# Optimization experiments

Hardware: AMD Instinct MI355X
Metric: run time of the kernel (lower is better)

Reference implementation:

```python
import jax, jax.numpy as jnp
import numpy as np

B, N, D, WIN = 2, 4096, 256, 16


def setup_inputs() -> dict:
    key = jax.random.key(0)
    ks = jax.random.split(key, 10)
    def lin(k, o, i):
        return 0.02 * jax.random.normal(k, (o, i), jnp.float32)
    W = N // WIN
    return {
        "x": 0.5 * jax.random.normal(ks[0], (B, N, D), jnp.float32),
        "embed_qk": jax.random.normal(ks[1], (3, B, W, WIN, WIN, 3), jnp.float32),
        "act_proj_w": lin(ks[2], D, D), "act_proj_b": jnp.zeros((D,), jnp.float32),
        "proj_ln_g": jnp.ones((D,), jnp.float32), "proj_ln_b": jnp.zeros((D,), jnp.float32),
        "conv_w": lin(ks[3], D, D), "conv_b": jnp.zeros((D,), jnp.float32),
        "q_w": lin(ks[4], D, D), "q_b": jnp.zeros((D,), jnp.float32),
        "k_w": lin(ks[5], D, D), "k_b": jnp.zeros((D,), jnp.float32),
        "p_w": lin(ks[6], 1, 3), "p_b": jnp.zeros((1,), jnp.float32),
        "lin_w": lin(ks[7], D, D), "lin_b": jnp.zeros((D,), jnp.float32),
        "norm_g": jnp.ones((D,), jnp.float32), "norm_b": jnp.zeros((D,), jnp.float32),
    }


def _ln(x, g, b, eps=1e-5):
    m = x.mean(-1, keepdims=True)
    v = ((x - m) ** 2).mean(-1, keepdims=True)
    return (x - m) * jax.lax.rsqrt(v + eps) * g + b


def reference(x, embed_qk, act_proj_w, act_proj_b, proj_ln_g, proj_ln_b,
              conv_w, conv_b, q_w, q_b, k_w, k_b, p_w, p_b,
              lin_w, lin_b, norm_g, norm_b):
    # MSMAttentionLayer: gated residual path
    act_res = jax.nn.silu(x @ act_proj_w.T + act_proj_b)          # (B,N,C)
    h = _ln(x, proj_ln_g, proj_ln_b)
    h = jax.nn.silu(h @ conv_w.T + conv_b)                        # 1x1 conv == per-token linear

    # MSMLMultiHeadAttention, stage=1 (window 4x4=16); N % 16 == 0 so add_row_num = 0
    q = jax.nn.elu(h @ q_w.T + q_b) + 1.0
    k = jax.nn.elu(h @ k_w.T + k_b) + 1.0
    v = h
    Bn, Nn, C = h.shape
    Wn = Nn // WIN
    q_win = q.reshape(Bn, Wn, WIN, C)
    k_win = k.reshape(Bn, Wn, WIN, C)
    v_win = v.reshape(Bn, Wn, WIN, C)
    # learned relative-position bias: Linear(3,1) on embed_qk[stage]
    p = (embed_qk[1] @ p_w.T + p_b)[..., 0]
    # second elu+1 feature map (applied on top of q/k which are already elu+1)
    phi_q = jax.nn.elu(q_win) + 1.0
    phi_k = jax.nn.elu(k_win) + 1.0
    # linear-attention style KV aggregation: reduces over windows w
    KV = jnp.einsum('bwmc,bwmd->bmcd', phi_k, v_win)
    att = jnp.einsum('bwnc,bmcd->bwnmd', phi_q, KV) + p[..., None]
    attn_out = att.reshape(Bn, -1, C)[:, :Nn, :]                  # (B,N,C)

    hid = (attn_out * act_res) @ lin_w.T + lin_b
    return _ln(hid + h, norm_g, norm_b)
```

## Files before the change

kernel.cpp:

```cpp
#include <hip/hip_runtime.h>


#define DIM 256
#define NTOK 4096

typedef __attribute__((ext_vector_type(8))) short short8;
typedef __attribute__((ext_vector_type(4))) short short4v;
typedef __attribute__((ext_vector_type(4))) float f32x4;

__device__ __forceinline__ float silu_f(float z) { return z / (1.f + __expf(-z)); }
__device__ __forceinline__ float elu2_f(float z) { return z > 0.f ? z + 2.f : __expf(z) + 1.f; }

__device__ __forceinline__ short f2bf(float f) {
    union { float f; unsigned u; } v; v.f = f;
    unsigned r = v.u + 0x7fffu + ((v.u >> 16) & 1u);
    return (short)(r >> 16);
}
__device__ __forceinline__ float bf2f(short s) {
    union { unsigned u; float f; } v; v.u = ((unsigned)(unsigned short)s) << 16;
    return v.f;
}
__device__ __forceinline__ short8 cvt8(const float* src) {
    const float4 a = *(const float4*)src;
    const float4 c = *(const float4*)(src + 4);
    short8 s;
    s[0] = f2bf(a.x); s[1] = f2bf(a.y); s[2] = f2bf(a.z); s[3] = f2bf(a.w);
    s[4] = f2bf(c.x); s[5] = f2bf(c.y); s[6] = f2bf(c.z); s[7] = f2bf(c.w);
    return s;
}
__device__ __forceinline__ void cast_chunk(const float* __restrict__ src, short* __restrict__ dst,
                                           int chunk, int tid) {
    const int base = chunk * 8192 + tid * 32;
    #pragma unroll
    for (int j = 0; j < 4; ++j)
        *(short8*)(dst + base + j * 8) = cvt8(src + base + j * 8);
}

__global__ __launch_bounds__(256) void fused_dual(
        const float* __restrict__ XF,
        const float* __restrict__ W0f, const float* __restrict__ b0, short* __restrict__ Y0,
        const float* __restrict__ W1f, const float* __restrict__ b1, short* __restrict__ Y1,
        const float* __restrict__ G, const float* __restrict__ Bt,
        const float* __restrict__ Wkf, short* __restrict__ WKB,
        const float* __restrict__ Wqf, short* __restrict__ WQB) {
    const int tid = threadIdx.x;
    if (blockIdx.x >= 64) {
        if (blockIdx.y == 0 && blockIdx.z == 0) {
            const int which = blockIdx.x - 64;
            if (which < 8) cast_chunk(Wkf, WKB, which, tid);
            else cast_chunk(Wqf, WQB, which - 8, tid);
        }
        return;
    }
    __shared__ __align__(16) short Xs[2][128 * 72];
    __shared__ __align__(16) short Ws[2][64 * 72];
    __shared__ float stats[128][2];
    const int zz = blockIdx.z;
    const float* Wf = zz ? W1f : W0f;
    const float* bias = zz ? b1 : b0;
    short* Y = zz ? Y1 : Y0;
    const int wv = tid >> 6, l = tid & 63;
    const int lr = l & 15, lk = l >> 4;
    const int r0 = blockIdx.x * 128, c0 = blockIdx.y * 64;
    const int wm = (wv >> 1) * 64, wn = (wv & 1) * 32;
    const int sr = tid >> 3, sc = (tid & 7) * 8;

    if (zz) {
        const int prow = tid >> 1, phalf = tid & 1;
        const float* src = XF + (size_t)(r0 + prow) * DIM + phalf * 128;
        float a1 = 0.f, a2 = 0.f;
        #pragma unroll 8
        for (int j = 0; j < 32; ++j) {
            const float4 v = *(const float4*)(src + j * 4);
            a1 += v.x + v.y + v.z + v.w;
            a2 += v.x * v.x + v.y * v.y + v.z * v.z + v.w * v.w;
        }
        a1 += __shfl_xor(a1, 1);
        a2 += __shfl_xor(a2, 1);
        if (!phalf) {
            const float mm = a1 * (1.f / DIM);
            stats[prow][0] = mm;
            stats[prow][1] = rsqrtf(a2 * (1.f / DIM) - mm * mm + 1e-5f);
        }
        __syncthreads();
    }

    f32x4 acc[4][2];
    #pragma unroll
    for (int i = 0; i < 4; ++i)
        #pragma unroll
        for (int j = 0; j < 2; ++j) acc[i][j] = (f32x4){0.f, 0.f, 0.f, 0.f};

    float4 xa[4][2], wa[2][2];
    #pragma unroll
    for (int p = 0; p < 4; ++p) {
        const float* src = XF + (size_t)(r0 + sr + p * 32) * DIM + sc;
        xa[p][0] = *(const float4*)src;
        xa[p][1] = *(const float4*)(src + 4);
    }
    #pragma unroll
    for (int p = 0; p < 2; ++p) {
        const float* src = Wf + (size_t)(c0 + sr + p * 32) * DIM + sc;
        wa[p][0] = *(const float4*)src;
        wa[p][1] = *(const float4*)(src + 4);
    }

    int buf = 0;
    for (int s = 0; s < 4; ++s) {
        const int kt = s * 64;
        if (zz) {
            const float4 g1 = *(const float4*)(G + kt + sc);
            const float4 g2 = *(const float4*)(G + kt + sc + 4);
            const float4 t1 = *(const float4*)(Bt + kt + sc);
            const float4 t2 = *(const float4*)(Bt + kt + sc + 4);
            const float gv[8] = {g1.x, g1.y, g1.z, g1.w, g2.x, g2.y, g2.z, g2.w};
            const float bv[8] = {t1.x, t1.y, t1.z, t1.w, t2.x, t2.y, t2.z, t2.w};
            #pragma unroll
            for (int p = 0; p < 4; ++p) {
                const int row = sr + p * 32;
                const float mm = stats[row][0], rs = stats[row][1];
                const float v[8] = {xa[p][0].x, xa[p][0].y, xa[p][0].z, xa[p][0].w,
                                    xa[p][1].x, xa[p][1].y, xa[p][1].z, xa[p][1].w};
                short8 sS;
                #pragma unroll
                for (int j = 0; j < 8; ++j) sS[j] = f2bf((v[j] - mm) * rs * gv[j] + bv[j]);
                *(short8*)&Xs[buf][row * 72 + sc] = sS;
            }
        } else {
            #pragma unroll
            for (int p = 0; p < 4; ++p) {
                const int row = sr + p * 32;
                const float v[8] = {xa[p][0].x, xa[p][0].y, xa[p][0].z, xa[p][0].w,
                                    xa[p][1].x, xa[p][1].y, xa[p][1].z, xa[p][1].w};
                short8 sS;
                #pragma unroll
                for (int j = 0; j < 8; ++j) sS[j] = f2bf(v[j]);
                *(short8*)&Xs[buf][row * 72 + sc] = sS;
            }
        }
        #pragma unroll
        for (int p = 0; p < 2; ++p) {
            const int row = sr + p * 32;
            const float v[8] = {wa[p][0].x, wa[p][0].y, wa[p][0].z, wa[p][0].w,
                                wa[p][1].x, wa[p][1].y, wa[p][1].z, wa[p][1].w};
            short8 sS;
            #pragma unroll
            for (int j = 0; j < 8; ++j) sS[j] = f2bf(v[j]);
            *(short8*)&Ws[buf][row * 72 + sc] = sS;
        }
        __syncthreads();
        if (s < 3) {
            const int ktn = kt + 64;
            #pragma unroll
            for (int p = 0; p < 4; ++p) {
                const float* src = XF + (size_t)(r0 + sr + p * 32) * DIM + ktn + sc;
                xa[p][0] = *(const float4*)src;
                xa[p][1] = *(const float4*)(src + 4);
            }
            #pragma unroll
            for (int p = 0; p < 2; ++p) {
                const float* src = Wf + (size_t)(c0 + sr + p * 32) * DIM + ktn + sc;
                wa[p][0] = *(const float4*)src;
                wa[p][1] = *(const float4*)(src + 4);
            }
        }
        #pragma unroll
        for (int kc = 0; kc < 2; ++kc) {
            short8 af[4], bfr[2];
            #pragma unroll
            for (int mi = 0; mi < 4; ++mi)
                af[mi] = *(const short8*)&Xs[buf][(wm + mi * 16 + lr) * 72 + kc * 32 + lk * 8];
            #pragma unroll
            for (int ni = 0; ni < 2; ++ni)
                bfr[ni] = *(const short8*)&Ws[buf][(wn + ni * 16 + lr) * 72 + kc * 32 + lk * 8];
            #pragma unroll
            for (int mi = 0; mi < 4; ++mi)
                #pragma unroll
                for (int ni = 0; ni < 2; ++ni)
                    acc[mi][ni] = __builtin_amdgcn_mfma_f32_16x16x32_bf16(af[mi], bfr[ni], acc[mi][ni], 0, 0, 0);
        }
        buf ^= 1;
    }
    #pragma unroll
    for (int mi = 0; mi < 4; ++mi)
        #pragma unroll
        for (int ni = 0; ni < 2; ++ni) {
            const int c = c0 + wn + ni * 16 + lr;
            const float bv2 = bias[c];
            #pragma unroll
            for (int i = 0; i < 4; ++i) {
                const int r = r0 + wm + mi * 16 + lk * 4 + i;
                Y[(size_t)r * DIM + c] = f2bf(silu_f(acc[mi][ni][i] + bv2));
            }
        }
}

__global__ __launch_bounds__(256) void gemm_kq(
        const short* __restrict__ H, const short* __restrict__ WKB, const float* __restrict__ bk, short* __restrict__ PK,
        const short* __restrict__ WQB, const float* __restrict__ bq, short* __restrict__ PQ) {
    __shared__ __align__(16) short Xs[2][128 * 72];
    __shared__ __align__(16) short Ws[2][64 * 72];
    const int bx = blockIdx.x;
    const bool isq = bx >= 64;
    const short* W = isq ? WQB : WKB;
    const float* bias = isq ? bq : bk;
    short* Y = isq ? PQ : PK;
    const int r0 = (isq ? bx - 64 : bx) * 128;
    const int c0 = blockIdx.y * 64;
    const int tid = threadIdx.x;
    const int wv = tid >> 6, l = tid & 63;
    const int lr = l & 15, lk = l >> 4;
    const int wm = (wv >> 1) * 64, wn = (wv & 1) * 32;
    const int sr = tid >> 3, sc = (tid & 7) * 8;

    int growA[4];
    #pragma unroll
    for (int p = 0; p < 4; ++p) {
        int grow = r0 + sr + p * 32;
        if (isq) grow = ((grow >> 8) << 12) + (grow & 255);
        growA[p] = grow;
    }

    f32x4 acc[4][2];
    #pragma unroll
    for (int i = 0; i < 4; ++i)
        #pragma unroll
        for (int j = 0; j < 2; ++j) acc[i][j] = (f32x4){0.f, 0.f, 0.f, 0.f};

    short8 xa[4], wa[2];
    #pragma unroll
    for (int p = 0; p < 4; ++p)
        xa[p] = *(const short8*)(H + (size_t)growA[p] * DIM + sc);
    #pragma unroll
    for (int p = 0; p < 2; ++p)
        wa[p] = *(const short8*)(W + (size_t)(c0 + sr + p * 32) * DIM + sc);

    int buf = 0;
    for (int s = 0; s < 4; ++s) {
        #pragma unroll
        for (int p = 0; p < 4; ++p)
            *(short8*)&Xs[buf][(sr + p * 32) * 72 + sc] = xa[p];
        #pragma unroll
        for (int p = 0; p < 2; ++p)
            *(short8*)&Ws[buf][(sr + p * 32) * 72 + sc] = wa[p];
        __syncthreads();
        if (s < 3) {
            const int ktn = (s + 1) * 64;
            #pragma unroll
            for (int p = 0; p < 4; ++p)
                xa[p] = *(const short8*)(H + (size_t)growA[p] * DIM + ktn + sc);
            #pragma unroll
            for (int p = 0; p < 2; ++p)
                wa[p] = *(const short8*)(W + (size_t)(c0 + sr + p * 32) * DIM + ktn + sc);
        }
        #pragma unroll
        for (int kc = 0; kc < 2; ++kc) {
            short8 af[4], bfr[2];
            #pragma unroll
            for (int mi = 0; mi < 4; ++mi)
                af[mi] = *(const short8*)&Xs[buf][(wm + mi * 16 + lr) * 72 + kc * 32 + lk * 8];
            #pragma unroll
            for (int ni = 0; ni < 2; ++ni)
                bfr[ni] = *(const short8*)&Ws[buf][(wn + ni * 16 + lr) * 72 + kc * 32 + lk * 8];
            #pragma unroll
            for (int mi = 0; mi < 4; ++mi)
                #pragma unroll
                for (int ni = 0; ni < 2; ++ni)
                    acc[mi][ni] = __builtin_amdgcn_mfma_f32_16x16x32_bf16(af[mi], bfr[ni], acc[mi][ni], 0, 0, 0);
        }
        buf ^= 1;
    }
    #pragma unroll
    for (int mi = 0; mi < 4; ++mi)
        #pragma unroll
        for (int ni = 0; ni < 2; ++ni) {
            const int c = c0 + wn + ni * 16 + lr;
            const float bv = bias[c];
            #pragma unroll
            for (int i = 0; i < 4; ++i) {
                const int r = r0 + wm + mi * 16 + lk * 4 + i;
                Y[(size_t)r * DIM + c] = f2bf(elu2_f(acc[mi][ni][i] + bv));
            }
        }
}

__global__ __launch_bounds__(256) void kv_mfma(const short* __restrict__ HB, const short* __restrict__ PK,
                                               short* __restrict__ KVT,
                                               const float* __restrict__ Wlf, short* __restrict__ WLB) {
    const int tid = threadIdx.x;
    if (blockIdx.x >= 32) {
        if (blockIdx.y == 0 && blockIdx.z == 0)
            cast_chunk(Wlf, WLB, blockIdx.x - 32, tid);
        return;
    }
    __shared__ __align__(16) short Hs[2][64 * 68];
    __shared__ __align__(16) short Ps[2][64 * 68];
    const int bm = blockIdx.x, b = bm >> 4, m = bm & 15;
    const int d0 = blockIdx.y * 64, c0 = blockIdx.z * 64;
    const int wv = tid >> 6, l = tid & 63;
    const int lr = l & 15, lk = l >> 4;
    const int wd = (wv >> 1) * 32, wc = (wv & 1) * 32;
    f32x4 acc[2][2];
    #pragma unroll
    for (int i = 0; i < 2; ++i)
        #pragma unroll
        for (int j = 0; j < 2; ++j) acc[i][j] = (f32x4){0.f, 0.f, 0.f, 0.f};
    const size_t hbase = (size_t)b * NTOK * DIM;
    const int sr = tid >> 3, sc = (tid & 7) * 8;

    short8 hv[2], pv[2];
    #pragma unroll
    for (int p = 0; p < 2; ++p) {
        const int w = sr + p * 32;
        const size_t gg = hbase + (size_t)(w * 16 + m) * DIM;
        hv[p] = *(const short8*)(HB + gg + d0 + sc);
        pv[p] = *(const short8*)(PK + gg + c0 + sc);
    }

    int buf = 0;
    for (int s = 0; s < 4; ++s) {
        #pragma unroll
        for (int p = 0; p < 2; ++p) {
            const int w = sr + p * 32;
            *(short4v*)&Hs[buf][w * 68 + sc]     = __builtin_shufflevector(hv[p], hv[p], 0, 1, 2, 3);
            *(short4v*)&Hs[buf][w * 68 + sc + 4] = __builtin_shufflevector(hv[p], hv[p], 4, 5, 6, 7);
            *(short4v*)&Ps[buf][w * 68 + sc]     = __builtin_shufflevector(pv[p], pv[p], 0, 1, 2, 3);
            *(short4v*)&Ps[buf][w * 68 + sc + 4] = __builtin_shufflevector(pv[p], pv[p], 4, 5, 6, 7);
        }
        __syncthreads();
        if (s < 3) {
            const int ktn = (s + 1) * 64;
            #pragma unroll
            for (int p = 0; p < 2; ++p) {
                const int w = sr + p * 32;
                const size_t gg = hbase + (size_t)((ktn + w) * 16 + m) * DIM;
                hv[p] = *(const short8*)(HB + gg + d0 + sc);
                pv[p] = *(const short8*)(PK + gg + c0 + sc);
            }
        }
        #pragma unroll
        for (int kc = 0; kc < 2; ++kc) {
            const int kb = kc * 32 + lk * 8;
            short8 af[2], bfr[2];
            #pragma unroll
            for (int di = 0; di < 2; ++di)
                #pragma unroll
                for (int i = 0; i < 8; ++i)
                    af[di][i] = Hs[buf][(kb + i) * 68 + wd + di * 16 + lr];
            #pragma unroll
            for (int ci = 0; ci < 2; ++ci)
                #pragma unroll
                for (int i = 0; i < 8; ++i)
                    bfr[ci][i] = Ps[buf][(kb + i) * 68 + wc + ci * 16 + lr];
            #pragma unroll
            for (int di = 0; di < 2; ++di)
                #pragma unroll
                for (int ci = 0; ci < 2; ++ci)
                    acc[di][ci] = __builtin_amdgcn_mfma_f32_16x16x32_bf16(af[di], bfr[ci], acc[di][ci], 0, 0, 0);
        }
        buf ^= 1;
    }
    #pragma unroll
    for (int di = 0; di < 2; ++di)
        #pragma unroll
        for (int ci = 0; ci < 2; ++ci)
            #pragma unroll
            for (int i = 0; i < 4; ++i) {
                const int d = d0 + wd + di * 16 + lk * 4 + i;
                const int c = c0 + wc + ci * 16 + lr;
                KVT[((size_t)bm * DIM + d) * DIM + c] = f2bf(acc[di][ci][i]);
            }
}

__global__ __launch_bounds__(256) void attlin(
        const short* __restrict__ PQ, const short* __restrict__ KVT,
        const float* __restrict__ emb, const float* __restrict__ pw, const float* __restrict__ pb,
        const short* __restrict__ AR,
        const short* __restrict__ WLB, const float* __restrict__ bl,
        const short* __restrict__ HB, const float* __restrict__ G, const float* __restrict__ Bt,
        float* __restrict__ Y) {
    __shared__ __align__(16) short Qs[32 * 264];
    __shared__ __align__(16) short AGs[32 * 264];
    __shared__ __align__(16) short Bs[2][256 * 72];
    __shared__ float s1buf[32][2];
    __shared__ float s2buf[32][2];
    const int tid = threadIdx.x;
    const int wv = tid >> 6, l = tid & 63;
    const int lr = l & 15, lk = l >> 4;
    const int bm = blockIdx.x, b = bm >> 4, m = bm & 15;
    const int q0 = blockIdx.y * 32;
    const int wq = (wv >> 1) * 16;
    const int wd = (wv & 1) * 32;
    const int sr = tid >> 3, sc = (tid & 7) * 8;

    #pragma unroll
    for (int p = 0; p < 4; ++p) {
        const int chunk = tid + p * 256;
        const int row = chunk >> 5, cc = (chunk & 31) * 8;
        *(short8*)&Qs[row * 264 + cc] = *(const short8*)(PQ + (size_t)(b * 256 + q0 + row) * DIM + cc);
    }

    f32x4 accA[4][2];
    #pragma unroll
    for (int i = 0; i < 4; ++i)
        #pragma unroll
        for (int j = 0; j < 2; ++j) accA[i][j] = (f32x4){0.f, 0.f, 0.f, 0.f};
    short8 bv8[8];
    #pragma unroll
    for (int p = 0; p < 8; ++p)
        bv8[p] = *(const short8*)(KVT + ((size_t)bm * DIM + sr + p * 32) * DIM + sc);
    int buf = 0;
    for (int s = 0; s < 4; ++s) {
        const int kt = s * 64;
        #pragma unroll
        for (int p = 0; p < 8; ++p)
            *(short8*)&Bs[buf][(sr + p * 32) * 72 + sc] = bv8[p];
        __syncthreads();
        if (s < 3) {
            const int ktn = kt + 64;
            #pragma unroll
            for (int p = 0; p < 8; ++p)
                bv8[p] = *(const short8*)(KVT + ((size_t)bm * DIM + sr + p * 32) * DIM + ktn + sc);
        }
        #pragma unroll
        for (int kc = 0; kc < 2; ++kc) {
            const short8 af = *(const short8*)&Qs[(wq + lr) * 264 + kt + kc * 32 + lk * 8];
            #pragma unroll
            for (int dc = 0; dc < 4; ++dc)
                #pragma unroll
                for (int ni = 0; ni < 2; ++ni) {
                    const short8 bfr = *(const short8*)&Bs[buf][(dc * 64 + wd + ni * 16 + lr) * 72 + kc * 32 + lk * 8];
                    accA[dc][ni] = __builtin_amdgcn_mfma_f32_16x16x32_bf16(af, bfr, accA[dc][ni], 0, 0, 0);
                }
        }
        buf ^= 1;
    }
    __syncthreads();
    {
        const float pw0 = pw[0], pw1 = pw[1], pw2 = pw[2], pbv = pb[0];
        #pragma unroll
        for (int i = 0; i < 4; ++i) {
            const int rloc = wq + lk * 4 + i;
            const int qr = q0 + rloc;
            const int widx = qr >> 4, nidx = qr & 15;
            const float* e = emb + ((((size_t)(2 + b) * 256 + widx) * 16 + nidx) * 16 + m) * 3;
            const float pv = e[0] * pw0 + e[1] * pw1 + e[2] * pw2 + pbv;
            const int t = qr * 16 + m;
            #pragma unroll
            for (int dc = 0; dc < 4; ++dc)
                #pragma unroll
                for (int ni = 0; ni < 2; ++ni) {
                    const int d = dc * 64 + wd + ni * 16 + lr;
                    const size_t o = ((size_t)b * NTOK + t) * DIM + d;
                    AGs[rloc * 264 + d] = f2bf((accA[dc][ni][i] + pv) * bf2f(AR[o]));
                }
        }
    }
    __syncthreads();

    const int wn2 = (wv & 1) * 128;
    f32x4 accB[8];
    #pragma unroll
    for (int i = 0; i < 8; ++i) accB[i] = (f32x4){0.f, 0.f, 0.f, 0.f};
    #pragma unroll
    for (int p = 0; p < 8; ++p)
        bv8[p] = *(const short8*)(WLB + (size_t)(sr + p * 32) * DIM + sc);
    buf = 0;
    for (int s = 0; s < 4; ++s) {
        const int kt = s * 64;
        #pragma unroll
        for (int p = 0; p < 8; ++p)
            *(short8*)&Bs[buf][(sr + p * 32) * 72 + sc] = bv8[p];
        __syncthreads();
        if (s < 3) {
            const int ktn = kt + 64;
            #pragma unroll
            for (int p = 0; p < 8; ++p)
                bv8[p] = *(const short8*)(WLB + (size_t)(sr + p * 32) * DIM + ktn + sc);
        }
        #pragma unroll
        for (int kc = 0; kc < 2; ++kc) {
            const short8 af = *(const short8*)&AGs[(wq + lr) * 264 + kt + kc * 32 + lk * 8];
            #pragma unroll
            for (int ni = 0; ni < 8; ++ni) {
                const short8 bfr = *(const short8*)&Bs[buf][(wn2 + ni * 16 + lr) * 72 + kc * 32 + lk * 8];
                accB[ni] = __builtin_amdgcn_mfma_f32_16x16x32_bf16(af, bfr, accB[ni], 0, 0, 0);
            }
        }
        buf ^= 1;
    }
    float s1[4] = {0.f, 0.f, 0.f, 0.f}, s2[4] = {0.f, 0.f, 0.f, 0.f};
    #pragma unroll
    for (int ni = 0; ni < 8; ++ni) {
        const int col = wn2 + ni * 16 + lr;
        const float bv = bl[col];
        #pragma unroll
        for (int i = 0; i < 4; ++i) {
            const int rloc = wq + lk * 4 + i;
            const int t = (q0 + rloc) * 16 + m;
            const float z = accB[ni][i] + bv + bf2f(HB[((size_t)b * NTOK + t) * DIM + col]);
            accB[ni][i] = z;
            s1[i] += z; s2[i] += z * z;
        }
    }
    #pragma unroll
    for (int o = 1; o < 16; o <<= 1) {
        #pragma unroll
        for (int i = 0; i < 4; ++i) {
            s1[i] += __shfl_xor(s1[i], o);
            s2[i] += __shfl_xor(s2[i], o);
        }
    }
    if (lr == 0) {
        #pragma unroll
        for (int i = 0; i < 4; ++i) {
            const int rloc = wq + lk * 4 + i;
            s1buf[rloc][wv & 1] = s1[i];
            s2buf[rloc][wv & 1] = s2[i];
        }
    }
    __syncthreads();
    float mean[4], rstd[4];
    #pragma unroll
    for (int i = 0; i < 4; ++i) {
        const int rloc = wq + lk * 4 + i;
        const float t1 = s1buf[rloc][0] + s1buf[rloc][1];
        const float t2 = s2buf[rloc][0] + s2buf[rloc][1];
        const float mm = t1 * (1.f / DIM);
        mean[i] = mm;
        rstd[i] = rsqrtf(t2 * (1.f / DIM) - mm * mm + 1e-5f);
    }
    #pragma unroll
    for (int ni = 0; ni < 8; ++ni) {
        const int col = wn2 + ni * 16 + lr;
        const float gv = G[col], bv2 = Bt[col];
        #pragma unroll
        for (int i = 0; i < 4; ++i) {
            const int rloc = wq + lk * 4 + i;
            const int t = (q0 + rloc) * 16 + m;
            Y[((size_t)b * NTOK + t) * DIM + col] = (accB[ni][i] - mean[i]) * rstd[i] * gv + bv2;
        }
    }
}

extern "C" void kernel_launch(void* const* d_in, const int* in_sizes, int n_in,
                              void* d_out, int out_size, void* d_ws, size_t ws_size,
                              hipStream_t stream) {
    const float* x   = (const float*)d_in[0];
    const float* emb = (const float*)d_in[1];
    const float* Wa  = (const float*)d_in[2];
    const float* ba  = (const float*)d_in[3];
    const float* lng = (const float*)d_in[4];
    const float* lnb = (const float*)d_in[5];
    const float* Wc  = (const float*)d_in[6];
    const float* bc  = (const float*)d_in[7];
    const float* Wq  = (const float*)d_in[8];
    const float* bq  = (const float*)d_in[9];
    const float* Wk  = (const float*)d_in[10];
    const float* bk  = (const float*)d_in[11];
    const float* pw  = (const float*)d_in[12];
    const float* pb  = (const float*)d_in[13];
    const float* Wl  = (const float*)d_in[14];
    const float* bl  = (const float*)d_in[15];
    const float* ng  = (const float*)d_in[16];
    const float* nb  = (const float*)d_in[17];

    char* ws = (char*)d_ws;
    const size_t MB = 1024 * 1024;
    short* h_bf   = (short*)(ws + 0 * MB);
    short* phik   = (short*)(ws + 4 * MB);
    short* phiq   = (short*)(ws + 8 * MB);
    short* kvT    = (short*)(ws + 9 * MB);
    short* act_bf = (short*)(ws + 13 * MB);
    short* Wk_bf  = (short*)(ws + 17 * MB);
    short* Wq_bf  = (short*)(ws + 17 * MB + 128 * 1024);
    short* Wl_bf  = (short*)(ws + 17 * MB + 256 * 1024);

    fused_dual<<<dim3(80, 4, 2), dim3(256), 0, stream>>>(x, Wa, ba, act_bf,
                                                         Wc, bc, h_bf, lng, lnb,
                                                         Wk, Wk_bf, Wq, Wq_bf);
    gemm_kq<<<dim3(68, 4), dim3(256), 0, stream>>>(h_bf, Wk_bf, bk, phik, Wq_bf, bq, phiq);
    kv_mfma<<<dim3(40, 4, 4), dim3(256), 0, stream>>>(h_bf, phik, kvT, Wl, Wl_bf);
    attlin<<<dim3(32, 8), dim3(256), 0, stream>>>(phiq, kvT, emb, pw, pb, act_bf, Wl_bf, bl,
                                                  h_bf, ng, nb, (float*)d_out);
}
```

Before: 53.39 us.

## Move act_proj GEMM into K/Q kernel and hoist Wl cast to first kernel

The first kernel now computes only the LayerNorm+conv GEMM (h), and the act_proj GEMM on x moves into the second kernel alongside the K/Q GEMMs. The Wl bf16 cast moves from kv_mfma into the first kernel. This rebalances block counts across launches: the first kernel shrinks from 640 to 352 blocks and the second grows from 272 to 528. That shortens the critical path to h, which the K/Q and KV stages depend on. The trade-off is a heavier second kernel with two code paths in one launch, which may raise register pressure.

```diff
diff --git a/kernel.cpp b/kernel.cpp
--- a/kernel.cpp
+++ b/kernel.cpp
@@ -36,36 +36,33 @@
         *(short8*)(dst + base + j * 8) = cvt8(src + base + j * 8);
 }
 
-__global__ __launch_bounds__(256) void fused_dual(
+__global__ __launch_bounds__(256) void gemm_h(
         const float* __restrict__ XF,
-        const float* __restrict__ W0f, const float* __restrict__ b0, short* __restrict__ Y0,
-        const float* __restrict__ W1f, const float* __restrict__ b1, short* __restrict__ Y1,
+        const float* __restrict__ Wcf, const float* __restrict__ bc, short* __restrict__ H,
         const float* __restrict__ G, const float* __restrict__ Bt,
         const float* __restrict__ Wkf, short* __restrict__ WKB,
-        const float* __restrict__ Wqf, short* __restrict__ WQB) {
+        const float* __restrict__ Wqf, short* __restrict__ WQB,
+        const float* __restrict__ Wlf, short* __restrict__ WLB) {
     const int tid = threadIdx.x;
     if (blockIdx.x >= 64) {
-        if (blockIdx.y == 0 && blockIdx.z == 0) {
+        if (blockIdx.y == 0) {
             const int which = blockIdx.x - 64;
             if (which < 8) cast_chunk(Wkf, WKB, which, tid);
-            else cast_chunk(Wqf, WQB, which - 8, tid);
+            else if (which < 16) cast_chunk(Wqf, WQB, which - 8, tid);
+            else cast_chunk(Wlf, WLB, which - 16, tid);
         }
         return;
     }
     __shared__ __align__(16) short Xs[2][128 * 72];
     __shared__ __align__(16) short Ws[2][64 * 72];
     __shared__ float stats[128][2];
-    const int zz = blockIdx.z;
-    const float* Wf = zz ? W1f : W0f;
-    const float* bias = zz ? b1 : b0;
-    short* Y = zz ? Y1 : Y0;
     const int wv = tid >> 6, l = tid & 63;
     const int lr = l & 15, lk = l >> 4;
     const int r0 = blockIdx.x * 128, c0 = blockIdx.y * 64;
     const int wm = (wv >> 1) * 64, wn = (wv & 1) * 32;
     const int sr = tid >> 3, sc = (tid & 7) * 8;
 
-    if (zz) {
+    {
         const int prow = tid >> 1, phalf = tid & 1;
         const float* src = XF + (size_t)(r0 + prow) * DIM + phalf * 128;
         float a1 = 0.f, a2 = 0.f;
@@ -100,7 +97,7 @@
     }
     #pragma unroll
     for (int p = 0; p < 2; ++p) {
-        const float* src = Wf + (size_t)(c0 + sr + p * 32) * DIM + sc;
+        const float* src = Wcf + (size_t)(c0 + sr + p * 32) * DIM + sc;
         wa[p][0] = *(const float4*)src;
         wa[p][1] = *(const float4*)(src + 4);
     }
@@ -108,7 +105,7 @@
     int buf = 0;
     for (int s = 0; s < 4; ++s) {
         const int kt = s * 64;
-        if (zz) {
+        {
             const float4 g1 = *(const float4*)(G + kt + sc);
             const float4 g2 = *(const float4*)(G + kt + sc + 4);
             const float4 t1 = *(const float4*)(Bt + kt + sc);
@@ -126,17 +123,6 @@
                 for (int j = 0; j < 8; ++j) sS[j] = f2bf((v[j] - mm) * rs * gv[j] + bv[j]);
                 *(short8*)&Xs[buf][row * 72 + sc] = sS;
             }
-        } else {
-            #pragma unroll
-            for (int p = 0; p < 4; ++p) {
-                const int row = sr + p * 32;
-                const float v[8] = {xa[p][0].x, xa[p][0].y, xa[p][0].z, xa[p][0].w,
-                                    xa[p][1].x, xa[p][1].y, xa[p][1].z, xa[p][1].w};
-                short8 sS;
-                #pragma unroll
-                for (int j = 0; j < 8; ++j) sS[j] = f2bf(v[j]);
-                *(short8*)&Xs[buf][row * 72 + sc] = sS;
-            }
         }
         #pragma unroll
         for (int p = 0; p < 2; ++p) {
@@ -159,7 +145,7 @@
             }
             #pragma unroll
             for (int p = 0; p < 2; ++p) {
-                const float* src = Wf + (size_t)(c0 + sr + p * 32) * DIM + ktn + sc;
+                const float* src = Wcf + (size_t)(c0 + sr + p * 32) * DIM + ktn + sc;
                 wa[p][0] = *(const float4*)src;
                 wa[p][1] = *(const float4*)(src + 4);
             }
@@ -186,26 +172,23 @@
         #pragma unroll
         for (int ni = 0; ni < 2; ++ni) {
             const int c = c0 + wn + ni * 16 + lr;
-            const float bv2 = bias[c];
+            const float bv2 = bc[c];
             #pragma unroll
             for (int i = 0; i < 4; ++i) {
                 const int r = r0 + wm + mi * 16 + lk * 4 + i;
-                Y[(size_t)r * DIM + c] = f2bf(silu_f(acc[mi][ni][i] + bv2));
-            }
-        }
-}
-
-__global__ __launch_bounds__(256) void gemm_kq(
+                H[(size_t)r * DIM + c] = f2bf(silu_f(acc[mi][ni][i] + bv2));
+            }
+        }
+}
+
+__global__ __launch_bounds__(256) void kq_act(
         const short* __restrict__ H, const short* __restrict__ WKB, const float* __restrict__ bk, short* __restrict__ PK,
-        const short* __restrict__ WQB, const float* __restrict__ bq, short* __restrict__ PQ) {
+        const short* __restrict__ WQB, const float* __restrict__ bq, short* __restrict__ PQ,
+        const float* __restrict__ XF, const float* __restrict__ Waf, const float* __restrict__ ba,
+        short* __restrict__ ACT) {
     __shared__ __align__(16) short Xs[2][128 * 72];
     __shared__ __align__(16) short Ws[2][64 * 72];
     const int bx = blockIdx.x;
-    const bool isq = bx >= 64;
-    const short* W = isq ? WQB : WKB;
-    const float* bias = isq ? bq : bk;
-    short* Y = isq ? PQ : PK;
-    const int r0 = (isq ? bx - 64 : bx) * 128;
     const int c0 = blockIdx.y * 64;
     const int tid = threadIdx.x;
     const int wv = tid >> 6, l = tid & 63;
@@ -213,6 +196,102 @@
     const int wm = (wv >> 1) * 64, wn = (wv & 1) * 32;
     const int sr = tid >> 3, sc = (tid & 7) * 8;
 
+    f32x4 acc[4][2];
+    #pragma unroll
+    for (int i = 0; i < 4; ++i)
+        #pragma unroll
+        for (int j = 0; j < 2; ++j) acc[i][j] = (f32x4){0.f, 0.f, 0.f, 0.f};
+
+    if (bx >= 68) {
+        const int r0 = (bx - 68) * 128;
+        float4 xa[4][2], wa[2][2];
+        #pragma unroll
+        for (int p = 0; p < 4; ++p) {
+            const float* src = XF + (size_t)(r0 + sr + p * 32) * DIM + sc;
+            xa[p][0] = *(const float4*)src;
+            xa[p][1] = *(const float4*)(src + 4);
+        }
+        #pragma unroll
+        for (int p = 0; p < 2; ++p) {
+            const float* src = Waf + (size_t)(c0 + sr + p * 32) * DIM + sc;
+            wa[p][0] = *(const float4*)src;
+            wa[p][1] = *(const float4*)(src + 4);
+        }
+        int buf = 0;
+        for (int s = 0; s < 4; ++s) {
+            #pragma unroll
+            for (int p = 0; p < 4; ++p) {
+                const int row = sr + p * 32;
+                const float v[8] = {xa[p][0].x, xa[p][0].y, xa[p][0].z, xa[p][0].w,
+                                    xa[p][1].x, xa[p][1].y, xa[p][1].z, xa[p][1].w};
+                short8 sS;
+                #pragma unroll
+                for (int j = 0; j < 8; ++j) sS[j] = f2bf(v[j]);
+                *(short8*)&Xs[buf][row * 72 + sc] = sS;
+            }
+            #pragma unroll
+            for (int p = 0; p < 2; ++p) {
+                const int row = sr + p * 32;
+                const float v[8] = {wa[p][0].x, wa[p][0].y, wa[p][0].z, wa[p][0].w,
+                                    wa[p][1].x, wa[p][1].y, wa[p][1].z, wa[p][1].w};
+                short8 sS;
+                #pragma unroll
+                for (int j = 0; j < 8; ++j) sS[j] = f2bf(v[j]);
+                *(short8*)&Ws[buf][row * 72 + sc] = sS;
+            }
+            __syncthreads();
+            if (s < 3) {
+                const int ktn = (s + 1) * 64;
+                #pragma unroll
+                for (int p = 0; p < 4; ++p) {
+                    const float* src = XF + (size_t)(r0 + sr + p * 32) * DIM + ktn + sc;
+                    xa[p][0] = *(const float4*)src;
+                    xa[p][1] = *(const float4*)(src + 4);
+                }
+                #pragma unroll
+                for (int p = 0; p < 2; ++p) {
+                    const float* src = Waf + (size_t)(c0 + sr + p * 32) * DIM + ktn + sc;
+                    wa[p][0] = *(const float4*)src;
+                    wa[p][1] = *(const float4*)(src + 4);
+                }
+            }
+            #pragma unroll
+            for (int kc = 0; kc < 2; ++kc) {
+                short8 af[4], bfr[2];
+                #pragma unroll
+                for (int mi = 0; mi < 4; ++mi)
+                    af[mi] = *(const short8*)&Xs[buf][(wm + mi * 16 + lr) * 72 + kc * 32 + lk * 8];
+                #pragma unroll
+                for (int ni = 0; ni < 2; ++ni)
+                    bfr[ni] = *(const short8*)&Ws[buf][(wn + ni * 16 + lr) * 72 + kc * 32 + lk * 8];
+                #pragma unroll
+                for (int mi = 0; mi < 4; ++mi)
+                    #pragma unroll
+                    for (int ni = 0; ni < 2; ++ni)
+                        acc[mi][ni] = __builtin_amdgcn_mfma_f32_16x16x32_bf16(af[mi], bfr[ni], acc[mi][ni], 0, 0, 0);
+            }
+            buf ^= 1;
+        }
+        #pragma unroll
+        for (int mi = 0; mi < 4; ++mi)
+            #pragma unroll
+            for (int ni = 0; ni < 2; ++ni) {
+                const int c = c0 + wn + ni * 16 + lr;
+                const float bv = ba[c];
+                #pragma unroll
+                for (int i = 0; i < 4; ++i) {
+                    const int r = r0 + wm + mi * 16 + lk * 4 + i;
+                    ACT[(size_t)r * DIM + c] = f2bf(silu_f(acc[mi][ni][i] + bv));
+                }
+            }
+        return;
+    }
+
+    const bool isq = bx >= 64;
+    const short* W = isq ? WQB : WKB;
+    const float* bias = isq ? bq : bk;
+    short* Y = isq ? PQ : PK;
+    const int r0 = (isq ? bx - 64 : bx) * 128;
     int growA[4];
     #pragma unroll
     for (int p = 0; p < 4; ++p) {
@@ -220,13 +299,6 @@
         if (isq) grow = ((grow >> 8) << 12) + (grow & 255);
         growA[p] = grow;
     }
-
-    f32x4 acc[4][2];
-    #pragma unroll
-    for (int i = 0; i < 4; ++i)
-        #pragma unroll
-        for (int j = 0; j < 2; ++j) acc[i][j] = (f32x4){0.f, 0.f, 0.f, 0.f};
-
     short8 xa[4], wa[2];
     #pragma unroll
     for (int p = 0; p < 4; ++p)
@@ -234,7 +306,6 @@
     #pragma unroll
     for (int p = 0; p < 2; ++p)
         wa[p] = *(const short8*)(W + (size_t)(c0 + sr + p * 32) * DIM + sc);
-
     int buf = 0;
     for (int s = 0; s < 4; ++s) {
         #pragma unroll
@@ -285,16 +356,10 @@
 }
 
 __global__ __launch_bounds__(256) void kv_mfma(const short* __restrict__ HB, const short* __restrict__ PK,
-                                               short* __restrict__ KVT,
-                                               const float* __restrict__ Wlf, short* __restrict__ WLB) {
-    const int tid = threadIdx.x;
-    if (blockIdx.x >= 32) {
-        if (blockIdx.y == 0 && blockIdx.z == 0)
-            cast_chunk(Wlf, WLB, blockIdx.x - 32, tid);
-        return;
-    }
+                                               short* __restrict__ KVT) {
     __shared__ __align__(16) short Hs[2][64 * 68];
     __shared__ __align__(16) short Ps[2][64 * 68];
+    const int tid = threadIdx.x;
     const int bm = blockIdx.x, b = bm >> 4, m = bm & 15;
     const int d0 = blockIdx.y * 64, c0 = blockIdx.z * 64;
     const int wv = tid >> 6, l = tid & 63;
@@ -576,11 +641,11 @@
     short* Wq_bf  = (short*)(ws + 17 * MB + 128 * 1024);
     short* Wl_bf  = (short*)(ws + 17 * MB + 256 * 1024);
 
-    fused_dual<<<dim3(80, 4, 2), dim3(256), 0, stream>>>(x, Wa, ba, act_bf,
-                                                         Wc, bc, h_bf, lng, lnb,
-                                                         Wk, Wk_bf, Wq, Wq_bf);
-    gemm_kq<<<dim3(68, 4), dim3(256), 0, stream>>>(h_bf, Wk_bf, bk, phik, Wq_bf, bq, phiq);
-    kv_mfma<<<dim3(40, 4, 4), dim3(256), 0, stream>>>(h_bf, phik, kvT, Wl, Wl_bf);
+    gemm_h<<<dim3(88, 4), dim3(256), 0, stream>>>(x, Wc, bc, h_bf, lng, lnb,
+                                                  Wk, Wk_bf, Wq, Wq_bf, Wl, Wl_bf);
+    kq_act<<<dim3(132, 4), dim3(256), 0, stream>>>(h_bf, Wk_bf, bk, phik, Wq_bf, bq, phiq,
+                                                   x, Wa, ba, act_bf);
+    kv_mfma<<<dim3(32, 4, 4), dim3(256), 0, stream>>>(h_bf, phik, kvT);
     attlin<<<dim3(32, 8), dim3(256), 0, stream>>>(phiq, kvT, emb, pw, pb, act_bf, Wl_bf, bl,
                                                   h_bf, ng, nb, (float*)d_out);
 }
```

New measurement: 55.40 us. +3.8%, slower.
